# Kernel tuning notes

Measured on AMD Instinct MI355X. Metric: run time of the kernel, lower is better.

The kernel has to match this reference:

```python
import jax, jax.numpy as jnp
import numpy as np

B = 64          # number of graphs
MAX_N = 2048    # nodes per graph (equal-sized for static shapes)
H = 128         # hidden_dim
C = 64          # num_clusters
THRESH = 0.75


def setup_inputs() -> dict:
    key = jax.random.key(0)
    ks = jax.random.split(key, 12)
    N = B * MAX_N
    x1 = jax.random.normal(ks[0], (N, H), jnp.float32)
    x2 = jax.random.normal(ks[1], (N, H), jnp.float32)
    # sorted graph-id vectors; equal-sized graphs keep dense shapes static
    batch1 = jnp.repeat(jnp.arange(B, dtype=jnp.int64), MAX_N)
    batch2 = jnp.repeat(jnp.arange(B, dtype=jnp.int64), MAX_N)
    # learned params (xavier-ish scale)
    s = 1.0 / np.sqrt(H)
    Q = jax.random.normal(ks[2], (1, C, H), jnp.float32) * s
    WQ_w = jax.random.normal(ks[3], (H, H), jnp.float32) * s
    WQ_b = jnp.zeros((H,), jnp.float32)
    WK_w = jax.random.normal(ks[4], (H, H), jnp.float32) * s
    WK_b = jnp.zeros((H,), jnp.float32)
    WV_w = jax.random.normal(ks[5], (H, H), jnp.float32) * s
    WV_b = jnp.zeros((H,), jnp.float32)
    WO_w = jax.random.normal(ks[6], (H, H), jnp.float32) * s
    WO_b = jnp.zeros((H,), jnp.float32)
    return {"x1": x1, "x2": x2, "batch1": batch1, "batch2": batch2,
            "Q": Q, "WQ_w": WQ_w, "WQ_b": WQ_b, "WK_w": WK_w, "WK_b": WK_b,
            "WV_w": WV_w, "WV_b": WV_b, "WO_w": WO_w, "WO_b": WO_b}


def _linear(x, w, b):
    # torch nn.Linear: y = x @ w.T + b
    return x @ w.T + b


def _to_dense_batch(x, batch):
    # [N, H] + sorted batch ids -> [B, MAX_N, H], bool mask [B, MAX_N]
    N = batch.shape[0]
    counts = jax.ops.segment_sum(jnp.ones_like(batch), batch, num_segments=B)
    starts = jnp.cumsum(counts) - counts               # exclusive prefix sum
    pos = jnp.arange(N) - starts[batch]                # intra-graph position
    dense = jnp.zeros((B, MAX_N, x.shape[-1]), x.dtype).at[batch, pos].set(x)
    mask = jnp.zeros((B, MAX_N), bool).at[batch, pos].set(True)
    return dense, mask


def _global_topk_mask(A):
    flat = A.reshape(-1)
    k = int(flat.shape[0] * THRESH)
    thr = jax.lax.top_k(flat, k)[0][-1]   # min of the top-k values
    return A * (A >= thr)


def reference(x1, x2, batch1, batch2, Q, WQ_w, WQ_b, WK_w, WK_b, WV_w, WV_b, WO_w, WO_b):
    K1, _ = _to_dense_batch(_linear(x1, WK_w, WK_b), batch1)   # [B, MAX_N, H]
    V1, _ = _to_dense_batch(_linear(x1, WV_w, WV_b), batch1)
    K2, _ = _to_dense_batch(_linear(x2, WK_w, WK_b), batch2)
    V2, _ = _to_dense_batch(_linear(x2, WV_w, WV_b), batch2)

    Qp = _linear(jnp.broadcast_to(Q, (B, C, H)), WQ_w, WQ_b)   # [B, C, H]
    scale = 1.0 / jnp.sqrt(jnp.asarray(H, jnp.float32))

    # scores [B, C, MAX_N]; softmax over the CLUSTER axis (dim=-2)
    A1 = jax.nn.softmax(jnp.einsum('bch,bnh->bcn', Qp, K2) * scale, axis=-2)
    A2 = jax.nn.softmax(jnp.einsum('bch,bnh->bcn', Qp, K1) * scale, axis=-2)

    A1 = _global_topk_mask(A1)
    A2 = _global_topk_mask(A2)

    out1 = jax.nn.relu(_linear(jnp.einsum('bcn,bnh->bch', A1, V2), WO_w, WO_b))
    out2 = jax.nn.relu(_linear(jnp.einsum('bcn,bnh->bch', A2, V1), WO_w, WO_b))
    return (out1, out2)
```

## Files before the change

kernel.cpp:

```cpp
#include <hip/hip_runtime.h>

namespace {

constexpr unsigned KRANK = 6291456u;
constexpr int TOT4 = 2097152;
constexpr float SCALE = 0.08838834764831845f;

__device__ __forceinline__ unsigned short f2bf(float v) {
  unsigned u = __float_as_uint(v);
  return (unsigned short)((u + 0x7FFFu + ((u >> 16) & 1u)) >> 16);
}
__device__ __forceinline__ float bf2f(unsigned short h) {
  return __uint_as_float(((unsigned)h) << 16);
}

__global__ __launch_bounds__(256) void k_prep1(
    const float* __restrict__ Q, const float* __restrict__ WQ_w,
    const float* __restrict__ WQ_b, const float* __restrict__ WO_w,
    const float* __restrict__ WV_w, const float* __restrict__ WV_b,
    float* __restrict__ Qp0, float* __restrict__ M, float* __restrict__ bo2) {
  int i = blockIdx.x * 256 + threadIdx.x;
  if (i < 8192) {
    int c = i >> 7, h = i & 127;
    float s = WQ_b[h];
    for (int j = 0; j < 128; ++j) s = fmaf(Q[c * 128 + j], WQ_w[h * 128 + j], s);
    Qp0[i] = s;
  } else if (i < 24576) {
    int ii = i - 8192;
    int o = ii >> 7, j = ii & 127;
    float s = 0.f;
    for (int h = 0; h < 128; ++h) s = fmaf(WO_w[o * 128 + h], WV_w[h * 128 + j], s);
    M[ii] = s;
  } else if (i < 24704) {
    int o = i - 24576;
    float s = 0.f;
    for (int h = 0; h < 128; ++h) s = fmaf(WO_w[o * 128 + h], WV_b[h], s);
    bo2[o] = s;
  }
}

__global__ __launch_bounds__(256) void k_prep2(
    const float* __restrict__ Qp0, const float* __restrict__ WK_w,
    const float* __restrict__ WK_b, float* __restrict__ QkT, float* __restrict__ qb) {
  int i = blockIdx.x * 256 + threadIdx.x;
  if (i < 8192) {
    int c = i >> 7, j = i & 127;
    float s = 0.f;
    for (int h = 0; h < 128; ++h) s = fmaf(Qp0[c * 128 + h], WK_w[h * 128 + j], s);
    QkT[((j >> 2) * 64 + c) * 4 + (j & 3)] = s * SCALE;
  } else if (i < 8256) {
    int c = i - 8192;
    float s = 0.f;
    for (int h = 0; h < 128; ++h) s = fmaf(Qp0[c * 128 + h], WK_b[h], s);
    qb[c] = s * SCALE;
  }
}

__global__ __launch_bounds__(256, 4) void k_scores(
    const float* __restrict__ x, const float4* __restrict__ QkT,
    const float* __restrict__ qb, float* __restrict__ A,
    unsigned* __restrict__ gh1) {
  __shared__ float4 q_s[2048];
  __shared__ float qb_s[64];
  int t = threadIdx.x;
  int row0 = blockIdx.x * 128;
  for (int i = t; i < 2048; i += 256) q_s[i] = QkT[i];
  if (t < 64) qb_s[t] = qb[t];
  __syncthreads();

  int cg = t & 7;
  int rq = t >> 3;
  const float4* x4 = (const float4*)x + (row0 + rq) * 32;

  float acc[4][8];
#pragma unroll
  for (int r = 0; r < 4; ++r)
#pragma unroll
    for (int u = 0; u < 8; ++u) acc[r][u] = 0.f;

#pragma unroll 2
  for (int jb = 0; jb < 32; ++jb) {
    float4 xv0 = x4[jb];
    float4 xv1 = x4[1024 + jb];
    float4 xv2 = x4[2048 + jb];
    float4 xv3 = x4[3072 + jb];
#pragma unroll
    for (int u = 0; u < 8; ++u) {
      float4 q = q_s[jb * 64 + cg + 8 * u];
      acc[0][u] = fmaf(xv0.w, q.w, fmaf(xv0.z, q.z, fmaf(xv0.y, q.y, fmaf(xv0.x, q.x, acc[0][u]))));
      acc[1][u] = fmaf(xv1.w, q.w, fmaf(xv1.z, q.z, fmaf(xv1.y, q.y, fmaf(xv1.x, q.x, acc[1][u]))));
      acc[2][u] = fmaf(xv2.w, q.w, fmaf(xv2.z, q.z, fmaf(xv2.y, q.y, fmaf(xv2.x, q.x, acc[2][u]))));
      acc[3][u] = fmaf(xv3.w, q.w, fmaf(xv3.z, q.z, fmaf(xv3.y, q.y, fmaf(xv3.x, q.x, acc[3][u]))));
    }
  }

  __syncthreads();
  unsigned* hh = (unsigned*)q_s;
  for (int i = t; i < 8192; i += 256) hh[i] = 0;
  __syncthreads();

  float4* A4 = (float4*)A;
#pragma unroll
  for (int r = 0; r < 4; ++r) {
    float m = -1e30f;
#pragma unroll
    for (int u = 0; u < 8; ++u) { acc[r][u] += qb_s[cg + 8 * u]; m = fmaxf(m, acc[r][u]); }
    m = fmaxf(m, __shfl_xor(m, 1));
    m = fmaxf(m, __shfl_xor(m, 2));
    m = fmaxf(m, __shfl_xor(m, 4));
    float p[8];
    float ss = 0.f;
#pragma unroll
    for (int u = 0; u < 8; ++u) { p[u] = __expf(acc[r][u] - m); ss += p[u]; }
    ss += __shfl_xor(ss, 1);
    ss += __shfl_xor(ss, 2);
    ss += __shfl_xor(ss, 4);
    float inv = 1.0f / ss;
    int rowg = row0 + rq + 32 * r;
    float4 s0, s1;
    s0.x = p[0] * inv; s0.y = p[1] * inv; s0.z = p[2] * inv; s0.w = p[3] * inv;
    s1.x = p[4] * inv; s1.y = p[5] * inv; s1.z = p[6] * inv; s1.w = p[7] * inv;
    A4[rowg * 16 + cg * 2] = s0;
    A4[rowg * 16 + cg * 2 + 1] = s1;
    atomicAdd(&hh[__float_as_uint(s0.x) >> 18], 1u);
    atomicAdd(&hh[__float_as_uint(s0.y) >> 18], 1u);
    atomicAdd(&hh[__float_as_uint(s0.z) >> 18], 1u);
    atomicAdd(&hh[__float_as_uint(s0.w) >> 18], 1u);
    atomicAdd(&hh[__float_as_uint(s1.x) >> 18], 1u);
    atomicAdd(&hh[__float_as_uint(s1.y) >> 18], 1u);
    atomicAdd(&hh[__float_as_uint(s1.z) >> 18], 1u);
    atomicAdd(&hh[__float_as_uint(s1.w) >> 18], 1u);
  }
  __syncthreads();
  for (int i = t; i < 8192; i += 256) {
    unsigned c = hh[i];
    if (c) atomicAdd(&gh1[i], c);
  }
}

__device__ __forceinline__ void rankfind(const unsigned* __restrict__ gh, int nb,
                                         unsigned K, unsigned& bin, unsigned& krem,
                                         unsigned* sh) {
  int t = threadIdx.x;
  int chunk = (nb >= 256) ? (nb >> 8) : 1;
  int nt = (nb >= 256) ? 256 : nb;
  unsigned s = 0;
  int base = nb - 1 - t * chunk;
  if (t < nt)
    for (int i = 0; i < chunk; ++i) s += gh[base - i];
  sh[t] = s;
  __syncthreads();
  for (int off = 1; off < 256; off <<= 1) {
    unsigned v = (t >= off) ? sh[t - off] : 0u;
    __syncthreads();
    sh[t] += v;
    __syncthreads();
  }
  unsigned inc = sh[t], before = inc - s;
  if (t < nt && before < K && K <= inc) {
    unsigned cum = before;
    for (int i = 0; i < chunk; ++i) {
      unsigned hb = gh[base - i];
      cum += hb;
      if (cum >= K) { sh[256] = (unsigned)(base - i); sh[257] = K - (cum - hb); break; }
    }
  }
  __syncthreads();
  bin = sh[256];
  krem = sh[257];
  __syncthreads();
}

__global__ __launch_bounds__(256) void k_sel(
    const unsigned* __restrict__ gh1, const unsigned* __restrict__ gh2,
    const unsigned* __restrict__ gh3, unsigned* __restrict__ st, int stage) {
  __shared__ unsigned sh[258];
  unsigned bin, krem;
  int t = threadIdx.x;
  if (stage == 0) {
    rankfind(gh1, 8192, KRANK, bin, krem, sh);
    if (t == 0) { st[0] = bin; st[1] = krem; }
  } else if (stage == 1) {
    rankfind(gh2, 2048, st[1], bin, krem, sh);
    if (t == 0) { st[2] = bin; st[3] = krem; st[4] = (st[0] << 11) | bin; }
  } else {
    rankfind(gh3, 128, st[3], bin, krem, sh);
    if (t == 0) st[5] = (st[0] << 18) | (st[2] << 7) | bin;
  }
}

__global__ __launch_bounds__(256) void k_h2(const uint4* __restrict__ A4,
                                            const unsigned* __restrict__ st,
                                            unsigned* __restrict__ gh2) {
  __shared__ unsigned hh[2048];
  unsigned pref = st[0];
  int t = threadIdx.x;
  for (int i = t; i < 2048; i += 256) hh[i] = 0;
  __syncthreads();
  for (int i = blockIdx.x * 256 + t; i < TOT4; i += 131072) {
    uint4 v = A4[i];
    unsigned vv[4] = {v.x, v.y, v.z, v.w};
#pragma unroll
    for (int q = 0; q < 4; ++q)
      if ((vv[q] >> 18) == pref) atomicAdd(&hh[(vv[q] >> 7) & 2047u], 1u);
  }
  __syncthreads();
  for (int i = t; i < 2048; i += 256) {
    unsigned c = hh[i];
    if (c) atomicAdd(&gh2[i], c);
  }
}

__global__ __launch_bounds__(256) void k_h3(const uint4* __restrict__ A4,
                                            const unsigned* __restrict__ st,
                                            unsigned* __restrict__ gh3) {
  __shared__ unsigned hh[128];
  unsigned pref = st[4];
  int t = threadIdx.x;
  if (t < 128) hh[t] = 0;
  __syncthreads();
  for (int i = blockIdx.x * 256 + t; i < TOT4; i += 131072) {
    uint4 v = A4[i];
    unsigned vv[4] = {v.x, v.y, v.z, v.w};
#pragma unroll
    for (int q = 0; q < 4; ++q)
      if ((vv[q] >> 7) == pref) atomicAdd(&hh[vv[q] & 127u], 1u);
  }
  __syncthreads();
  if (t < 128) {
    unsigned c = hh[t];
    if (c) atomicAdd(&gh3[t], c);
  }
}

__global__ __launch_bounds__(256, 3) void k_tmat(
    const float* __restrict__ A, const float* __restrict__ x,
    const unsigned* __restrict__ st, unsigned short* __restrict__ Tp,
    float* __restrict__ rp, int nch) {
  __shared__ float4 smem[3200];
  __shared__ float rm[64];
  float4* as0 = smem;
  float4* as1 = smem + 544;
  float4* xs0 = smem + 1088;
  float4* xs1 = smem + 2144;
  int t = threadIdx.x;
  if (t < 64) rm[t] = 0.f;
  float thr = __uint_as_float(st[5]);
  int b = blockIdx.x / nch, chunk = blockIdx.x - b * nch;
  int nper = 2048 / nch;
  int subs = nper >> 5;
  int n0 = b * 2048 + chunk * nper;
  int na = t >> 4, c4 = t & 15;
  int nx = t >> 5, jx = t & 31;
  int h = t >> 7, ht = t & 127;
  int cg = ht >> 4, jg = ht & 15;
  const float4* Ag4 = (const float4*)A;
  const float4* Xg4 = (const float4*)x;

  float4 acc[8][2];
#pragma unroll
  for (int c = 0; c < 8; ++c) { acc[c][0] = make_float4(0, 0, 0, 0); acc[c][1] = make_float4(0, 0, 0, 0); }
  float4 racc = make_float4(0, 0, 0, 0);
  float4 ar0, ar1, xr0, xr1, xr2, xr3;

  auto gload = [&](int sub) {
    int nb = n0 + sub * 32;
    ar0 = Ag4[(nb + na) * 16 + c4];
    ar1 = Ag4[(nb + na + 16) * 16 + c4];
    xr0 = Xg4[(nb + nx) * 32 + jx];
    xr1 = Xg4[(nb + nx + 8) * 32 + jx];
    xr2 = Xg4[(nb + nx + 16) * 32 + jx];
    xr3 = Xg4[(nb + nx + 24) * 32 + jx];
  };
  auto maskw = [&](int buf) {
    float4* as = buf ? as1 : as0;
    float4* xs = buf ? xs1 : xs0;
    ar0.x = (ar0.x >= thr) ? ar0.x : 0.f;
    ar0.y = (ar0.y >= thr) ? ar0.y : 0.f;
    ar0.z = (ar0.z >= thr) ? ar0.z : 0.f;
    ar0.w = (ar0.w >= thr) ? ar0.w : 0.f;
    ar1.x = (ar1.x >= thr) ? ar1.x : 0.f;
    ar1.y = (ar1.y >= thr) ? ar1.y : 0.f;
    ar1.z = (ar1.z >= thr) ? ar1.z : 0.f;
    ar1.w = (ar1.w >= thr) ? ar1.w : 0.f;
    racc.x += ar0.x + ar1.x;
    racc.y += ar0.y + ar1.y;
    racc.z += ar0.z + ar1.z;
    racc.w += ar0.w + ar1.w;
    as[na * 17 + c4] = ar0;
    as[(na + 16) * 17 + c4] = ar1;
    xs[nx * 33 + jx] = xr0;
    xs[(nx + 8) * 33 + jx] = xr1;
    xs[(nx + 16) * 33 + jx] = xr2;
    xs[(nx + 24) * 33 + jx] = xr3;
  };

  gload(0);
  maskw(0);
  for (int sub = 0; sub < subs; ++sub) {
    int cur = sub & 1;
    __syncthreads();
    if (sub + 1 < subs) gload(sub + 1);
    const float4* as = cur ? as1 : as0;
    const float4* xs = cur ? xs1 : xs0;
    int nbase = h * 16;
#pragma unroll 4
    for (int k = 0; k < 16; ++k) {
      int n = nbase + k;
      float4 a0 = as[n * 17 + cg * 2];
      float4 a1 = as[n * 17 + cg * 2 + 1];
      float4 x0 = xs[n * 33 + jg * 2];
      float4 x1 = xs[n * 33 + jg * 2 + 1];
      float av[8] = {a0.x, a0.y, a0.z, a0.w, a1.x, a1.y, a1.z, a1.w};
#pragma unroll
      for (int c = 0; c < 8; ++c) {
        acc[c][0].x = fmaf(av[c], x0.x, acc[c][0].x);
        acc[c][0].y = fmaf(av[c], x0.y, acc[c][0].y);
        acc[c][0].z = fmaf(av[c], x0.z, acc[c][0].z);
        acc[c][0].w = fmaf(av[c], x0.w, acc[c][0].w);
        acc[c][1].x = fmaf(av[c], x1.x, acc[c][1].x);
        acc[c][1].y = fmaf(av[c], x1.y, acc[c][1].y);
        acc[c][1].z = fmaf(av[c], x1.z, acc[c][1].z);
        acc[c][1].w = fmaf(av[c], x1.w, acc[c][1].w);
      }
    }
    if (sub + 1 < subs) maskw(cur ^ 1);
  }

  __syncthreads();
  float4* am4 = smem;
  if (h == 0) {
#pragma unroll
    for (int c = 0; c < 8; ++c) {
      am4[(cg * 8 + c) * 32 + jg * 2] = acc[c][0];
      am4[(cg * 8 + c) * 32 + jg * 2 + 1] = acc[c][1];
    }
  }
  __syncthreads();
  if (h == 1) {
#pragma unroll
    for (int c = 0; c < 8; ++c) {
      int i0 = (cg * 8 + c) * 32 + jg * 2;
      float4 v0 = am4[i0], v1 = am4[i0 + 1];
      v0.x += acc[c][0].x; v0.y += acc[c][0].y; v0.z += acc[c][0].z; v0.w += acc[c][0].w;
      v1.x += acc[c][1].x; v1.y += acc[c][1].y; v1.z += acc[c][1].z; v1.w += acc[c][1].w;
      am4[i0] = v0; am4[i0 + 1] = v1;
    }
  }
  __syncthreads();
  ushort4* Tp4 = (ushort4*)Tp;
  size_t tb = (size_t)(b * nch + chunk) * 2048;
  for (int i = t; i < 2048; i += 256) {
    float4 v = smem[i];
    ushort4 o;
    o.x = f2bf(v.x); o.y = f2bf(v.y); o.z = f2bf(v.z); o.w = f2bf(v.w);
    Tp4[tb + i] = o;
  }
  atomicAdd(&rm[c4 * 4 + 0], racc.x);
  atomicAdd(&rm[c4 * 4 + 1], racc.y);
  atomicAdd(&rm[c4 * 4 + 2], racc.z);
  atomicAdd(&rm[c4 * 4 + 3], racc.w);
  __syncthreads();
  if (t < 64) rp[(b * nch + chunk) * 64 + t] = rm[t];
}

__global__ __launch_bounds__(256, 1) void k_final(
    const unsigned short* __restrict__ Tp, const float* __restrict__ rp,
    const float* __restrict__ M, const float* __restrict__ bo2,
    const float* __restrict__ WO_b, float* __restrict__ out, int nch) {
  __shared__ float m_s[128 * 132];
  __shared__ float t_s[16 * 132];
  __shared__ float r_s[16];
  __shared__ float b2_s[128], wb_s[128];
  int t = threadIdx.x;
  int b = blockIdx.x >> 2, chq = blockIdx.x & 3;
  const float4* Mg = (const float4*)M;
  float4* ms4 = (float4*)m_s;
  for (int i = t; i < 4096; i += 256) { int o = i >> 5, j4 = i & 31; ms4[o * 33 + j4] = Mg[i]; }
  const ushort4* Tp4 = (const ushort4*)Tp;
  int c0 = t >> 5, j40 = t & 31;
  float4 s0 = make_float4(0, 0, 0, 0), s1 = make_float4(0, 0, 0, 0);
  for (int ch = 0; ch < nch; ++ch) {
    size_t base = (size_t)(b * nch + ch) * 2048 + (size_t)(chq * 16) * 32;
    ushort4 u0 = Tp4[base + c0 * 32 + j40];
    ushort4 u1 = Tp4[base + (c0 + 8) * 32 + j40];
    s0.x += bf2f(u0.x); s0.y += bf2f(u0.y); s0.z += bf2f(u0.z); s0.w += bf2f(u0.w);
    s1.x += bf2f(u1.x); s1.y += bf2f(u1.y); s1.z += bf2f(u1.z); s1.w += bf2f(u1.w);
  }
  float4* ts4 = (float4*)t_s;
  ts4[c0 * 33 + j40] = s0;
  ts4[(c0 + 8) * 33 + j40] = s1;
  if (t < 16) {
    float rs = 0.f;
    for (int ch = 0; ch < nch; ++ch) rs += rp[(b * nch + ch) * 64 + chq * 16 + t];
    r_s[t] = rs;
  }
  if (t < 128) { b2_s[t] = bo2[t]; wb_s[t] = WO_b[t]; }
  __syncthreads();
  int og = t & 15, cq = t >> 4;
  float acc[8] = {0, 0, 0, 0, 0, 0, 0, 0};
  const float4* t4 = (const float4*)t_s;
  const float4* m4 = (const float4*)m_s;
  for (int jb = 0; jb < 32; ++jb) {
    float4 tv = t4[cq * 33 + jb];
#pragma unroll
    for (int u = 0; u < 8; ++u) {
      float4 mv = m4[(og + 16 * u) * 33 + jb];
      acc[u] = fmaf(tv.w, mv.w, fmaf(tv.z, mv.z, fmaf(tv.y, mv.y, fmaf(tv.x, mv.x, acc[u]))));
    }
  }
  int cp = chq * 16 + cq;
  int ctrue = (cp >> 3) + 8 * (cp & 7);
#pragma unroll
  for (int u = 0; u < 8; ++u) {
    int o = og + 16 * u;
    float v = acc[u] + r_s[cq] * b2_s[o] + wb_s[o];
    out[b * 8192 + ctrue * 128 + o] = fmaxf(v, 0.f);
  }
}

}

extern "C" void kernel_launch(void* const* d_in, const int* in_sizes, int n_in,
                              void* d_out, int out_size, void* d_ws, size_t ws_size,
                              hipStream_t stream) {
  (void)in_sizes; (void)n_in; (void)out_size;
  const float* x1   = (const float*)d_in[0];
  const float* x2   = (const float*)d_in[1];
  const float* Q    = (const float*)d_in[4];
  const float* WQ_w = (const float*)d_in[5];
  const float* WQ_b = (const float*)d_in[6];
  const float* WK_w = (const float*)d_in[7];
  const float* WK_b = (const float*)d_in[8];
  const float* WV_w = (const float*)d_in[9];
  const float* WV_b = (const float*)d_in[10];
  const float* WO_w = (const float*)d_in[11];
  const float* WO_b = (const float*)d_in[12];
  float* out = (float*)d_out;
  char* ws = (char*)d_ws;

  auto padsz = [](size_t x) { return (x + 255) & ~(size_t)255; };
  int nch = 16;
  for (;;) {
    size_t tot = padsz(33554432) + padsz((size_t)nch * 1048576) +
                 padsz((size_t)nch * 16384) + padsz(32768) + padsz(8192) +
                 padsz(1024) + padsz(256) + padsz(32768) + padsz(256) +
                 padsz(65536) + padsz(512);
    if (tot <= ws_size || nch == 2) break;
    nch >>= 1;
  }

  size_t off = 0;
  auto alloc = [&](size_t bytes) { size_t o = off; off += (bytes + 255) & ~(size_t)255; return o; };
  size_t A_off   = alloc(33554432);
  size_t Tp_off  = alloc((size_t)nch * 1048576);
  size_t rp_off  = alloc((size_t)nch * 16384);
  size_t h1_off  = alloc(32768);
  size_t h2_off  = alloc(8192);
  size_t h3_off  = alloc(1024);
  size_t zone_end = off;
  size_t st_off  = alloc(256);
  size_t QkT_off = alloc(32768);
  size_t qb_off  = alloc(256);
  size_t M_off   = alloc(65536);
  size_t bo2_off = alloc(512);

  float* A = (float*)(ws + A_off);
  unsigned short* Tp = (unsigned short*)(ws + Tp_off);
  float* rp = (float*)(ws + rp_off);
  unsigned* gh1 = (unsigned*)(ws + h1_off);
  unsigned* gh2 = (unsigned*)(ws + h2_off);
  unsigned* gh3 = (unsigned*)(ws + h3_off);
  unsigned* st  = (unsigned*)(ws + st_off);
  float* Qp0 = (float*)(ws + Tp_off);
  float* QkT = (float*)(ws + QkT_off);
  float* qb  = (float*)(ws + qb_off);
  float* Mm  = (float*)(ws + M_off);
  float* bo2 = (float*)(ws + bo2_off);

  k_prep1<<<97, 256, 0, stream>>>(Q, WQ_w, WQ_b, WO_w, WV_w, WV_b, Qp0, Mm, bo2);
  k_prep2<<<33, 256, 0, stream>>>(Qp0, WK_w, WK_b, QkT, qb);

  for (int ten = 0; ten < 2; ++ten) {
    const float* x = ten ? x1 : x2;
    hipMemsetAsync(ws + h1_off, 0, zone_end - h1_off, stream);
    k_scores<<<1024, 256, 0, stream>>>(x, (const float4*)QkT, qb, A, gh1);
    k_sel<<<1, 256, 0, stream>>>(gh1, gh2, gh3, st, 0);
    k_h2<<<512, 256, 0, stream>>>((const uint4*)A, st, gh2);
    k_sel<<<1, 256, 0, stream>>>(gh1, gh2, gh3, st, 1);
    k_h3<<<512, 256, 0, stream>>>((const uint4*)A, st, gh3);
    k_sel<<<1, 256, 0, stream>>>(gh1, gh2, gh3, st, 2);
    k_tmat<<<64 * nch, 256, 0, stream>>>(A, x, st, Tp, rp, nch);
    k_final<<<256, 256, 0, stream>>>(Tp, rp, Mm, bo2, WO_b, out + ten * 524288, nch);
  }
}
```

Before: 446.6 us.

## Batch both attention branches into single launches and collapse radix select to two passes

Processes the x1 and x2 branches together in each kernel launch (doubling grid sizes) when the workspace is large enough, instead of running the pipeline twice serially. The three-pass radix select becomes two passes by using a 262144-bin global histogram with direct global atomics, which removes the k_h3 pass over A. It also software-prefetches the next x row chunk in k_scores and changes the tmat chunk count from 16 to 4. Costs are a doubled workspace, more contended global atomics in k_h2, and a larger memset and rankfind scan.

```diff
diff --git a/kernel.cpp b/kernel.cpp
--- a/kernel.cpp
+++ b/kernel.cpp
@@ -57,13 +57,18 @@
 }
 
 __global__ __launch_bounds__(256, 4) void k_scores(
-    const float* __restrict__ x, const float4* __restrict__ QkT,
-    const float* __restrict__ qb, float* __restrict__ A,
-    unsigned* __restrict__ gh1) {
+    const float* __restrict__ x0p, const float* __restrict__ x1p,
+    const float4* __restrict__ QkT, const float* __restrict__ qb,
+    float* __restrict__ A, unsigned* __restrict__ gh1) {
   __shared__ float4 q_s[2048];
   __shared__ float qb_s[64];
   int t = threadIdx.x;
-  int row0 = blockIdx.x * 128;
+  int e = (blockIdx.x >= 1024) ? 1 : 0;
+  const float* x = e ? x1p : x0p;
+  int row0 = (blockIdx.x - (e << 10)) * 128;
+  float* Ae = A + (size_t)e * 8388608;
+  unsigned* gh1e = gh1 + e * 8192;
+
   for (int i = t; i < 2048; i += 256) q_s[i] = QkT[i];
   if (t < 64) qb_s[t] = qb[t];
   __syncthreads();
@@ -78,20 +83,22 @@
 #pragma unroll
     for (int u = 0; u < 8; ++u) acc[r][u] = 0.f;
 
-#pragma unroll 2
+  float4 cv0 = x4[0], cv1 = x4[1024], cv2 = x4[2048], cv3 = x4[3072];
   for (int jb = 0; jb < 32; ++jb) {
-    float4 xv0 = x4[jb];
-    float4 xv1 = x4[1024 + jb];
-    float4 xv2 = x4[2048 + jb];
-    float4 xv3 = x4[3072 + jb];
+    int nj = (jb + 1) & 31;
+    float4 nv0 = x4[nj];
+    float4 nv1 = x4[1024 + nj];
+    float4 nv2 = x4[2048 + nj];
+    float4 nv3 = x4[3072 + nj];
 #pragma unroll
     for (int u = 0; u < 8; ++u) {
       float4 q = q_s[jb * 64 + cg + 8 * u];
-      acc[0][u] = fmaf(xv0.w, q.w, fmaf(xv0.z, q.z, fmaf(xv0.y, q.y, fmaf(xv0.x, q.x, acc[0][u]))));
-      acc[1][u] = fmaf(xv1.w, q.w, fmaf(xv1.z, q.z, fmaf(xv1.y, q.y, fmaf(xv1.x, q.x, acc[1][u]))));
-      acc[2][u] = fmaf(xv2.w, q.w, fmaf(xv2.z, q.z, fmaf(xv2.y, q.y, fmaf(xv2.x, q.x, acc[2][u]))));
-      acc[3][u] = fmaf(xv3.w, q.w, fmaf(xv3.z, q.z, fmaf(xv3.y, q.y, fmaf(xv3.x, q.x, acc[3][u]))));
-    }
+      acc[0][u] = fmaf(cv0.w, q.w, fmaf(cv0.z, q.z, fmaf(cv0.y, q.y, fmaf(cv0.x, q.x, acc[0][u]))));
+      acc[1][u] = fmaf(cv1.w, q.w, fmaf(cv1.z, q.z, fmaf(cv1.y, q.y, fmaf(cv1.x, q.x, acc[1][u]))));
+      acc[2][u] = fmaf(cv2.w, q.w, fmaf(cv2.z, q.z, fmaf(cv2.y, q.y, fmaf(cv2.x, q.x, acc[2][u]))));
+      acc[3][u] = fmaf(cv3.w, q.w, fmaf(cv3.z, q.z, fmaf(cv3.y, q.y, fmaf(cv3.x, q.x, acc[3][u]))));
+    }
+    cv0 = nv0; cv1 = nv1; cv2 = nv2; cv3 = nv3;
   }
 
   __syncthreads();
@@ -99,7 +106,7 @@
   for (int i = t; i < 8192; i += 256) hh[i] = 0;
   __syncthreads();
 
-  float4* A4 = (float4*)A;
+  float4* A4 = (float4*)Ae;
 #pragma unroll
   for (int r = 0; r < 4; ++r) {
     float m = -1e30f;
@@ -134,7 +141,7 @@
   __syncthreads();
   for (int i = t; i < 8192; i += 256) {
     unsigned c = hh[i];
-    if (c) atomicAdd(&gh1[i], c);
+    if (c) atomicAdd(&gh1e[i], c);
   }
 }
 
@@ -173,88 +180,67 @@
 
 __global__ __launch_bounds__(256) void k_sel(
     const unsigned* __restrict__ gh1, const unsigned* __restrict__ gh2,
-    const unsigned* __restrict__ gh3, unsigned* __restrict__ st, int stage) {
+    unsigned* __restrict__ st, int stage) {
   __shared__ unsigned sh[258];
+  int e = blockIdx.x;
+  unsigned* ste = st + e * 64;
   unsigned bin, krem;
   int t = threadIdx.x;
   if (stage == 0) {
-    rankfind(gh1, 8192, KRANK, bin, krem, sh);
-    if (t == 0) { st[0] = bin; st[1] = krem; }
-  } else if (stage == 1) {
-    rankfind(gh2, 2048, st[1], bin, krem, sh);
-    if (t == 0) { st[2] = bin; st[3] = krem; st[4] = (st[0] << 11) | bin; }
+    rankfind(gh1 + e * 8192, 8192, KRANK, bin, krem, sh);
+    if (t == 0) { ste[0] = bin; ste[1] = krem; }
   } else {
-    rankfind(gh3, 128, st[3], bin, krem, sh);
-    if (t == 0) st[5] = (st[0] << 18) | (st[2] << 7) | bin;
+    rankfind(gh2 + (size_t)e * 262144, 262144, ste[1], bin, krem, sh);
+    if (t == 0) ste[5] = (ste[0] << 18) | bin;
   }
 }
 
 __global__ __launch_bounds__(256) void k_h2(const uint4* __restrict__ A4,
                                             const unsigned* __restrict__ st,
                                             unsigned* __restrict__ gh2) {
-  __shared__ unsigned hh[2048];
-  unsigned pref = st[0];
-  int t = threadIdx.x;
-  for (int i = t; i < 2048; i += 256) hh[i] = 0;
-  __syncthreads();
-  for (int i = blockIdx.x * 256 + t; i < TOT4; i += 131072) {
-    uint4 v = A4[i];
+  int e = (blockIdx.x >= 512) ? 1 : 0;
+  const uint4* Ae = A4 + (size_t)e * TOT4;
+  unsigned pref = st[e * 64];
+  unsigned* gh2e = gh2 + (size_t)e * 262144;
+  int t = threadIdx.x;
+  for (int i = (blockIdx.x - (e << 9)) * 256 + t; i < TOT4; i += 131072) {
+    uint4 v = Ae[i];
     unsigned vv[4] = {v.x, v.y, v.z, v.w};
 #pragma unroll
     for (int q = 0; q < 4; ++q)
-      if ((vv[q] >> 18) == pref) atomicAdd(&hh[(vv[q] >> 7) & 2047u], 1u);
-  }
-  __syncthreads();
-  for (int i = t; i < 2048; i += 256) {
-    unsigned c = hh[i];
-    if (c) atomicAdd(&gh2[i], c);
-  }
-}
-
-__global__ __launch_bounds__(256) void k_h3(const uint4* __restrict__ A4,
-                                            const unsigned* __restrict__ st,
-                                            unsigned* __restrict__ gh3) {
-  __shared__ unsigned hh[128];
-  unsigned pref = st[4];
-  int t = threadIdx.x;
-  if (t < 128) hh[t] = 0;
-  __syncthreads();
-  for (int i = blockIdx.x * 256 + t; i < TOT4; i += 131072) {
-    uint4 v = A4[i];
-    unsigned vv[4] = {v.x, v.y, v.z, v.w};
-#pragma unroll
-    for (int q = 0; q < 4; ++q)
-      if ((vv[q] >> 7) == pref) atomicAdd(&hh[vv[q] & 127u], 1u);
-  }
-  __syncthreads();
-  if (t < 128) {
-    unsigned c = hh[t];
-    if (c) atomicAdd(&gh3[t], c);
+      if ((vv[q] >> 18) == pref) atomicAdd(&gh2e[vv[q] & 0x3FFFFu], 1u);
   }
 }
 
 __global__ __launch_bounds__(256, 3) void k_tmat(
-    const float* __restrict__ A, const float* __restrict__ x,
-    const unsigned* __restrict__ st, unsigned short* __restrict__ Tp,
-    float* __restrict__ rp, int nch) {
+    const float* __restrict__ A, const float* __restrict__ x0p,
+    const float* __restrict__ x1p, const unsigned* __restrict__ st,
+    unsigned short* __restrict__ Tp, float* __restrict__ rp,
+    int lnch, int pten) {
   __shared__ float4 smem[3200];
   __shared__ float rm[64];
+  int t = threadIdx.x;
+  if (t < 64) rm[t] = 0.f;
+  int e = (blockIdx.x >= pten) ? 1 : 0;
+  int idx = blockIdx.x - e * pten;
+  const float* x = e ? x1p : x0p;
+  const float* Ae = A + (size_t)e * 8388608;
+  float thr = __uint_as_float(st[e * 64 + 5]);
+  int nch = 1 << lnch;
+  int b = idx >> lnch, chunk = idx & (nch - 1);
+  int nper = 2048 >> lnch;
+  int subs = nper >> 5;
+  int n0 = b * 2048 + chunk * nper;
+
   float4* as0 = smem;
   float4* as1 = smem + 544;
   float4* xs0 = smem + 1088;
   float4* xs1 = smem + 2144;
-  int t = threadIdx.x;
-  if (t < 64) rm[t] = 0.f;
-  float thr = __uint_as_float(st[5]);
-  int b = blockIdx.x / nch, chunk = blockIdx.x - b * nch;
-  int nper = 2048 / nch;
-  int subs = nper >> 5;
-  int n0 = b * 2048 + chunk * nper;
   int na = t >> 4, c4 = t & 15;
   int nx = t >> 5, jx = t & 31;
   int h = t >> 7, ht = t & 127;
   int cg = ht >> 4, jg = ht & 15;
-  const float4* Ag4 = (const float4*)A;
+  const float4* Ag4 = (const float4*)Ae;
   const float4* Xg4 = (const float4*)x;
 
   float4 acc[8][2];
@@ -349,7 +335,7 @@
   }
   __syncthreads();
   ushort4* Tp4 = (ushort4*)Tp;
-  size_t tb = (size_t)(b * nch + chunk) * 2048;
+  size_t tb = ((size_t)(e * 64 + b) * (size_t)nch + chunk) * 2048;
   for (int i = t; i < 2048; i += 256) {
     float4 v = smem[i];
     ushort4 o;
@@ -361,19 +347,22 @@
   atomicAdd(&rm[c4 * 4 + 2], racc.z);
   atomicAdd(&rm[c4 * 4 + 3], racc.w);
   __syncthreads();
-  if (t < 64) rp[(b * nch + chunk) * 64 + t] = rm[t];
+  if (t < 64) rp[((size_t)(e * 64 + b) * (size_t)nch + chunk) * 64 + t] = rm[t];
 }
 
 __global__ __launch_bounds__(256, 1) void k_final(
     const unsigned short* __restrict__ Tp, const float* __restrict__ rp,
     const float* __restrict__ M, const float* __restrict__ bo2,
-    const float* __restrict__ WO_b, float* __restrict__ out, int nch) {
+    const float* __restrict__ WO_b, float* __restrict__ out, int lnch) {
   __shared__ float m_s[128 * 132];
   __shared__ float t_s[16 * 132];
   __shared__ float r_s[16];
   __shared__ float b2_s[128], wb_s[128];
   int t = threadIdx.x;
-  int b = blockIdx.x >> 2, chq = blockIdx.x & 3;
+  int e = (blockIdx.x >= 256) ? 1 : 0;
+  int idx = blockIdx.x - (e << 8);
+  int b = idx >> 2, chq = idx & 3;
+  int nch = 1 << lnch;
   const float4* Mg = (const float4*)M;
   float4* ms4 = (float4*)m_s;
   for (int i = t; i < 4096; i += 256) { int o = i >> 5, j4 = i & 31; ms4[o * 33 + j4] = Mg[i]; }
@@ -381,7 +370,7 @@
   int c0 = t >> 5, j40 = t & 31;
   float4 s0 = make_float4(0, 0, 0, 0), s1 = make_float4(0, 0, 0, 0);
   for (int ch = 0; ch < nch; ++ch) {
-    size_t base = (size_t)(b * nch + ch) * 2048 + (size_t)(chq * 16) * 32;
+    size_t base = ((size_t)(e * 64 + b) * (size_t)nch + ch) * 2048 + (size_t)(chq * 16) * 32;
     ushort4 u0 = Tp4[base + c0 * 32 + j40];
     ushort4 u1 = Tp4[base + (c0 + 8) * 32 + j40];
     s0.x += bf2f(u0.x); s0.y += bf2f(u0.y); s0.z += bf2f(u0.z); s0.w += bf2f(u0.w);
@@ -392,7 +381,8 @@
   ts4[(c0 + 8) * 33 + j40] = s1;
   if (t < 16) {
     float rs = 0.f;
-    for (int ch = 0; ch < nch; ++ch) rs += rp[(b * nch + ch) * 64 + chq * 16 + t];
+    for (int ch = 0; ch < nch; ++ch)
+      rs += rp[((size_t)(e * 64 + b) * (size_t)nch + ch) * 64 + chq * 16 + t];
     r_s[t] = rs;
   }
   if (t < 128) { b2_s[t] = bo2[t]; wb_s[t] = WO_b[t]; }
@@ -415,7 +405,7 @@
   for (int u = 0; u < 8; ++u) {
     int o = og + 16 * u;
     float v = acc[u] + r_s[cq] * b2_s[o] + wb_s[o];
-    out[b * 8192 + ctrue * 128 + o] = fmaxf(v, 0.f);
+    out[(size_t)e * 524288 + b * 8192 + ctrue * 128 + o] = fmaxf(v, 0.f);
   }
 }
 
@@ -440,39 +430,41 @@
   char* ws = (char*)d_ws;
 
   auto padsz = [](size_t x) { return (x + 255) & ~(size_t)255; };
-  int nch = 16;
-  for (;;) {
-    size_t tot = padsz(33554432) + padsz((size_t)nch * 1048576) +
-                 padsz((size_t)nch * 16384) + padsz(32768) + padsz(8192) +
-                 padsz(1024) + padsz(256) + padsz(32768) + padsz(256) +
-                 padsz(65536) + padsz(512);
-    if (tot <= ws_size || nch == 2) break;
-    nch >>= 1;
-  }
+  auto need = [&](int nt, int nc) {
+    return padsz((size_t)nt * 33554432) + padsz((size_t)nt * nc * 1048576) +
+           padsz((size_t)nt * nc * 16384) + padsz((size_t)nt * 32768) +
+           padsz((size_t)nt * 1048576) + padsz((size_t)nt * 256) +
+           padsz(32768) + padsz(32768) + padsz(256) + padsz(65536) + padsz(512);
+  };
+  int nten, lnch;
+  if (ws_size >= need(2, 4))      { nten = 2; lnch = 2; }
+  else if (ws_size >= need(1, 8)) { nten = 1; lnch = 3; }
+  else                            { nten = 1; lnch = 2; }
+  int nch = 1 << lnch;
 
   size_t off = 0;
   auto alloc = [&](size_t bytes) { size_t o = off; off += (bytes + 255) & ~(size_t)255; return o; };
-  size_t A_off   = alloc(33554432);
-  size_t Tp_off  = alloc((size_t)nch * 1048576);
-  size_t rp_off  = alloc((size_t)nch * 16384);
-  size_t h1_off  = alloc(32768);
-  size_t h2_off  = alloc(8192);
-  size_t h3_off  = alloc(1024);
+  size_t A_off   = alloc((size_t)nten * 33554432);
+  size_t Tp_off  = alloc((size_t)nten * nch * 1048576);
+  size_t rp_off  = alloc((size_t)nten * nch * 16384);
+  size_t h1_off  = alloc((size_t)nten * 32768);
+  size_t h2_off  = alloc((size_t)nten * 1048576);
   size_t zone_end = off;
-  size_t st_off  = alloc(256);
+  size_t st_off  = alloc((size_t)nten * 256);
+  size_t Qp0_off = alloc(32768);
   size_t QkT_off = alloc(32768);
   size_t qb_off  = alloc(256);
   size_t M_off   = alloc(65536);
   size_t bo2_off = alloc(512);
+  (void)rp_off;
 
   float* A = (float*)(ws + A_off);
   unsigned short* Tp = (unsigned short*)(ws + Tp_off);
   float* rp = (float*)(ws + rp_off);
   unsigned* gh1 = (unsigned*)(ws + h1_off);
   unsigned* gh2 = (unsigned*)(ws + h2_off);
-  unsigned* gh3 = (unsigned*)(ws + h3_off);
   unsigned* st  = (unsigned*)(ws + st_off);
-  float* Qp0 = (float*)(ws + Tp_off);
+  float* Qp0 = (float*)(ws + Qp0_off);
   float* QkT = (float*)(ws + QkT_off);
   float* qb  = (float*)(ws + qb_off);
   float* Mm  = (float*)(ws + M_off);
@@ -481,16 +473,26 @@
   k_prep1<<<97, 256, 0, stream>>>(Q, WQ_w, WQ_b, WO_w, WV_w, WV_b, Qp0, Mm, bo2);
   k_prep2<<<33, 256, 0, stream>>>(Qp0, WK_w, WK_b, QkT, qb);
 
-  for (int ten = 0; ten < 2; ++ten) {
-    const float* x = ten ? x1 : x2;
+  if (nten == 2) {
+    int pten = 64 * nch;
     hipMemsetAsync(ws + h1_off, 0, zone_end - h1_off, stream);
-    k_scores<<<1024, 256, 0, stream>>>(x, (const float4*)QkT, qb, A, gh1);
-    k_sel<<<1, 256, 0, stream>>>(gh1, gh2, gh3, st, 0);
-    k_h2<<<512, 256, 0, stream>>>((const uint4*)A, st, gh2);
-    k_sel<<<1, 256, 0, stream>>>(gh1, gh2, gh3, st, 1);
-    k_h3<<<512, 256, 0, stream>>>((const uint4*)A, st, gh3);
-    k_sel<<<1, 256, 0, stream>>>(gh1, gh2, gh3, st, 2);
-    k_tmat<<<64 * nch, 256, 0, stream>>>(A, x, st, Tp, rp, nch);
-    k_final<<<256, 256, 0, stream>>>(Tp, rp, Mm, bo2, WO_b, out + ten * 524288, nch);
-  }
-}
+    k_scores<<<2048, 256, 0, stream>>>(x2, x1, (const float4*)QkT, qb, A, gh1);
+    k_sel<<<2, 256, 0, stream>>>(gh1, gh2, st, 0);
+    k_h2<<<1024, 256, 0, stream>>>((const uint4*)A, st, gh2);
+    k_sel<<<2, 256, 0, stream>>>(gh1, gh2, st, 1);
+    k_tmat<<<2 * pten, 256, 0, stream>>>(A, x2, x1, st, Tp, rp, lnch, pten);
+    k_final<<<512, 256, 0, stream>>>(Tp, rp, Mm, bo2, WO_b, out, lnch);
+  } else {
+    int pten = 64 * nch;
+    for (int ten = 0; ten < 2; ++ten) {
+      const float* x = ten ? x1 : x2;
+      hipMemsetAsync(ws + h1_off, 0, zone_end - h1_off, stream);
+      k_scores<<<1024, 256, 0, stream>>>(x, x, (const float4*)QkT, qb, A, gh1);
+      k_sel<<<1, 256, 0, stream>>>(gh1, gh2, st, 0);
+      k_h2<<<512, 256, 0, stream>>>((const uint4*)A, st, gh2);
+      k_sel<<<1, 256, 0, stream>>>(gh1, gh2, st, 1);
+      k_tmat<<<pten, 256, 0, stream>>>(A, x, x, st, Tp, rp, lnch, pten);
+      k_final<<<256, 256, 0, stream>>>(Tp, rp, Mm, bo2, WO_b, out + (size_t)ten * 524288, lnch);
+    }
+  }
+}
```

New measurement: 474.3 us. +6.2%, slower.
